# Kernel optimization log

Measured on AMD Instinct MI355X. Metric: run time of the kernel, lower is better.

Reference implementation:

```python
import jax, jax.numpy as jnp
import numpy as np

N, E, H, NH, S, EF, K = 25000, 400000, 64, 4, 16, 8, 2
HS = H // NH  # head size


def _ln(x, w, b):
    m = x.mean(-1, keepdims=True)
    v = ((x - m) ** 2).mean(-1, keepdims=True)
    return (x - m) / jnp.sqrt(v + 1e-5) * w + b


def _seg_softmax(scores, seg, n):
    # scores: [E, NH], seg: [E] -> softmax over edges sharing the same dest node
    mx = jax.ops.segment_max(scores, seg, num_segments=n)
    e = jnp.exp(scores - mx[seg])
    s = jax.ops.segment_sum(e, seg, num_segments=n)
    return e / (s[seg] + 1e-9)


def _edge_layer(h, x_s, src, dest, ef, w1, w2, proj, gated):
    # h: [N,H] (already layer-normed). Gather, fused per-edge MLP (no bias).
    inp = jnp.concatenate([h[src], h[dest], x_s[src], x_s[dest], ef], axis=-1)  # [E,168]
    raw = jnp.maximum(inp @ w1.T, 0.0) @ w2.T  # [E,NH]
    if gated:
        w = jax.nn.sigmoid(raw)
    else:
        w = _seg_softmax(jax.nn.leaky_relu(raw) / jnp.sqrt(jnp.asarray(HS, raw.dtype)), dest, N)
    msg = h.reshape(N, NH, HS)[src] * w[:, :, None]          # [E,NH,HS]
    agg = jax.ops.segment_sum(msg, dest, num_segments=N)     # [N,NH,HS]
    return agg.reshape(N, H) @ proj.T, w


def _mlp(x, w1, b1, w2, b2):
    return jnp.maximum(x @ w1.T + b1, 0.0) @ w2.T + b2


def _forward(x, x_s, edge_features, fwd_w1, fwd_w2, fwd_proj, rev_w1, rev_w2, rev_proj,
             ln_w, ln_b, r_w1, r_b1, r_w2, r_b2, z_w1, z_b1, z_w2, z_b2,
             c_w1, c_b1, c_w2, c_b2, edge_index):
    src, dest = edge_index[0], edge_index[1]
    # forward-direction stacked attention hops
    h_fwd, fwd_ws = x, []
    for k in range(K):
        h_norm = _ln(h_fwd, ln_w, ln_b)
        msg, w = _edge_layer(h_norm, x_s, src, dest, edge_features,
                             fwd_w1[k], fwd_w2[k], fwd_proj[k], gated=False)
        h_fwd = h_fwd + msg
        fwd_ws.append(w)
    fwd_ws = jnp.stack(fwd_ws, axis=-1)  # [E,NH,K]
    # reverse-direction stacked gating hops (edge direction flipped)
    h_rev, rev_ws = x, []
    for k in range(K):
        h_norm = _ln(h_rev, ln_w, ln_b)
        msg, w = _edge_layer(h_norm, x_s, dest, src, edge_features,
                             rev_w1[k], rev_w2[k], rev_proj[k], gated=True)
        h_rev = h_rev + msg
        rev_ws.append(w)
    rev_ws = jnp.stack(rev_ws, axis=-1)  # [E,NH,K]
    messages = jnp.concatenate([h_fwd - x, h_rev - x], axis=-1)  # [N,2H]
    gate_input = jnp.concatenate([x, messages], axis=-1)          # [N,3H]
    r_gate = jax.nn.sigmoid(_mlp(gate_input, r_w1, r_b1, r_w2, r_b2))
    z_gate = jax.nn.sigmoid(_mlp(gate_input, z_w1, z_b1, z_w2, z_b2))
    cand_in = jnp.concatenate([r_gate * x, messages], axis=-1)
    cand = jnp.tanh(_mlp(cand_in, c_w1, c_b1, c_w2, c_b2))
    final_h = (1.0 - z_gate) * x + z_gate * cand
    return final_h, fwd_ws, rev_ws, z_gate, r_gate


def setup_inputs() -> dict:
    key = jax.random.key(0)
    ks = jax.random.split(key, 20)
    mlp_in = 2 * H + 2 * S + EF  # 168
    width = 2 * H                # 128
    gi, gw = 3 * H, 3 * H        # 192, 192

    def nrm(k, shape, fan_in):
        return jax.random.normal(k, shape, jnp.float32) / np.sqrt(fan_in)

    return {
        'x': jax.random.normal(ks[0], (N, H), jnp.float32),
        'x_s': jax.random.normal(ks[1], (N, S), jnp.float32),
        'edge_index': jax.random.randint(ks[2], (2, E), 0, N, jnp.int32),
        'edge_features': jax.random.normal(ks[3], (E, EF), jnp.float32),
        'fwd_w1': nrm(ks[4], (K, width, mlp_in), mlp_in),
        'fwd_w2': nrm(ks[5], (K, NH, width), width),
        'fwd_proj': nrm(ks[6], (K, H, H), H),
        'rev_w1': nrm(ks[7], (K, width, mlp_in), mlp_in),
        'rev_w2': nrm(ks[8], (K, NH, width), width),
        'rev_proj': nrm(ks[9], (K, H, H), H),
        'ln_w': jnp.ones((H,), jnp.float32),
        'ln_b': jnp.zeros((H,), jnp.float32),
        'r_w1': nrm(ks[10], (gw, gi), gi), 'r_b1': jnp.zeros((gw,), jnp.float32),
        'r_w2': nrm(ks[11], (H, gw), gw), 'r_b2': jnp.zeros((H,), jnp.float32),
        'z_w1': nrm(ks[12], (gw, gi), gi), 'z_b1': jnp.zeros((gw,), jnp.float32),
        'z_w2': nrm(ks[13], (H, gw), gw), 'z_b2': jnp.zeros((H,), jnp.float32),
        'c_w1': nrm(ks[14], (gw, gi), gi), 'c_b1': jnp.zeros((gw,), jnp.float32),
        'c_w2': nrm(ks[15], (H, gw), gw), 'c_b2': jnp.zeros((H,), jnp.float32),
    }


def reference(x, x_s, edge_index, edge_features, fwd_w1, fwd_w2, fwd_proj,
              rev_w1, rev_w2, rev_proj, ln_w, ln_b, r_w1, r_b1, r_w2, r_b2,
              z_w1, z_b1, z_w2, z_b2, c_w1, c_b1, c_w2, c_b2):
    return _forward(x, x_s, edge_features, fwd_w1, fwd_w2, fwd_proj,
                    rev_w1, rev_w2, rev_proj, ln_w, ln_b,
                    r_w1, r_b1, r_w2, r_b2, z_w1, z_b1, z_w2, z_b2,
                    c_w1, c_b1, c_w2, c_b2, edge_index)
```

## Files before the change

### kernel.cpp

```cpp
#include <hip/hip_runtime.h>
#include <hip/hip_fp16.h>
#include <math.h>

#define NN 25000
#define EE 400000
#define HH 64
#define NHEAD 4
#define SDIM 16
#define EFDIM 8
#define KHOP 2
#define MIN 168
#define WID 128
#define GIN 192
#define KP 96

typedef __attribute__((ext_vector_type(8))) short bf16x8;
typedef __attribute__((ext_vector_type(4))) float f32x4;
typedef unsigned short ushortT;
typedef unsigned int uintT;

__device__ __forceinline__ float wave_sum64(float v) {
#pragma unroll
  for (int m = 1; m <= 32; m <<= 1) v += __shfl_xor(v, m, 64);
  return v;
}

__device__ __forceinline__ ushortT f2b(float f) {
  uintT u = __float_as_uint(f);
  return (ushortT)((u + 0x7FFFu + ((u >> 16) & 1u)) >> 16);
}
__device__ __forceinline__ float b2f(ushortT h) {
  return __uint_as_float(((uintT)h) << 16);
}

union U4H8 {
  uint4 u;
  __half2 h[4];
};

__device__ __forceinline__ __half2 relu2(__half2 v) {
  union { __half2 h; uintT u; } x;
  x.h = v;
  uintT mask = ((x.u & 0x80008000u) >> 15) * 0xFFFFu;
  x.u &= ~mask;
  return x.h;
}

__global__ void k_histo2(const int* __restrict__ src, const int* __restrict__ dst,
                         int* __restrict__ cnt_s, int* __restrict__ cnt_d) {
  int e = blockIdx.x * 256 + threadIdx.x;
  if (e < EE) {
    atomicAdd(&cnt_d[dst[e]], 1);
    atomicAdd(&cnt_s[src[e]], 1);
  }
}

__global__ void k_scan2(const int* __restrict__ cnt_d, const int* __restrict__ cnt_s,
                        int* __restrict__ rp_d, int* __restrict__ rp_s) {
  const int* cnt = blockIdx.x ? cnt_s : cnt_d;
  int* rp = blockIdx.x ? rp_s : rp_d;
  __shared__ int part[1024];
  int t = threadIdx.x;
  const int CH = (NN + 1023) / 1024;
  int base = t * CH;
  int s = 0;
  for (int i = 0; i < CH; ++i) {
    int j = base + i;
    if (j < NN) s += cnt[j];
  }
  part[t] = s;
  __syncthreads();
  for (int off = 1; off < 1024; off <<= 1) {
    int v = (t >= off) ? part[t - off] : 0;
    __syncthreads();
    part[t] += v;
    __syncthreads();
  }
  int run = (t == 0) ? 0 : part[t - 1];
  for (int i = 0; i < CH; ++i) {
    int j = base + i;
    if (j < NN) { rp[j] = run; run += cnt[j]; }
  }
  if (t == 1023) rp[NN] = run;
}

__global__ void k_scatter2(const int* __restrict__ src, const int* __restrict__ dst,
                           const int* __restrict__ rp_s, const int* __restrict__ rp_d,
                           int* __restrict__ cur_s, int* __restrict__ cur_d,
                           int* __restrict__ eid_s, int* __restrict__ eid_d) {
  int e = blockIdx.x * 256 + threadIdx.x;
  if (e < EE) {
    int nd = dst[e];
    int pd = atomicAdd(&cur_d[nd], 1);
    eid_d[rp_d[nd] + pd] = e;
    int ns = src[e];
    int ps = atomicAdd(&cur_s[ns], 1);
    eid_s[rp_s[ns] + ps] = e;
  }
}

__global__ __launch_bounds__(256) void k_sortseg2(const int* __restrict__ rp_d,
                                                  const int* __restrict__ rp_s,
                                                  int* __restrict__ eid_d,
                                                  int* __restrict__ eid_s) {
  int gw = blockIdx.x * 4 + (threadIdx.x >> 6);
  int lane = threadIdx.x & 63;
  if (gw >= 2 * NN) return;
  const int* rp = (gw < NN) ? rp_d : rp_s;
  int* eids = (gw < NN) ? eid_d : eid_s;
  int node = (gw < NN) ? gw : gw - NN;
  int beg = rp[node], end = rp[node + 1];
  int deg = end - beg;
  if (deg <= 1) return;
  if (deg <= 64) {
    int v = (lane < deg) ? eids[beg + lane] : 0x7fffffff;
#pragma unroll
    for (int k = 2; k <= 64; k <<= 1) {
#pragma unroll
      for (int j = k >> 1; j > 0; j >>= 1) {
        int other = __shfl_xor(v, j, 64);
        bool takeMin = (((lane & k) == 0) == ((lane & j) == 0));
        v = takeMin ? min(v, other) : max(v, other);
      }
    }
    if (lane < deg) eids[beg + lane] = v;
  } else if (lane == 0) {
    for (int i = beg + 1; i < end; ++i) {
      int v = eids[i];
      int j = i - 1;
      while (j >= beg && eids[j] > v) { eids[j + 1] = eids[j]; --j; }
      eids[j + 1] = v;
    }
  }
}

__global__ void k_mkpos2(const int* __restrict__ eid_d, const int* __restrict__ eid_s,
                         const int* __restrict__ src, const int* __restrict__ dst,
                         const float* __restrict__ ef, int4* __restrict__ pos_f,
                         int4* __restrict__ pos_r, uint4* __restrict__ efh_f,
                         uint4* __restrict__ efh_r) {
  int i = blockIdx.x * 256 + threadIdx.x;
  if (i >= EE) return;
  int e1 = eid_d[i];
  pos_f[i] = make_int4(e1, src[e1], dst[e1], 0);
  int e2 = eid_s[i];
  pos_r[i] = make_int4(e2, dst[e2], src[e2], 0);
  {
    float4 a0 = *(const float4*)(ef + (size_t)e1 * EFDIM);
    float4 a1 = *(const float4*)(ef + (size_t)e1 * EFDIM + 4);
    U4H8 u;
    u.h[0] = __floats2half2_rn(a0.x, a0.y);
    u.h[1] = __floats2half2_rn(a0.z, a0.w);
    u.h[2] = __floats2half2_rn(a1.x, a1.y);
    u.h[3] = __floats2half2_rn(a1.z, a1.w);
    efh_f[i] = u.u;
  }
  {
    float4 b0 = *(const float4*)(ef + (size_t)e2 * EFDIM);
    float4 b1 = *(const float4*)(ef + (size_t)e2 * EFDIM + 4);
    U4H8 u;
    u.h[0] = __floats2half2_rn(b0.x, b0.y);
    u.h[1] = __floats2half2_rn(b0.z, b0.w);
    u.h[2] = __floats2half2_rn(b1.x, b1.y);
    u.h[3] = __floats2half2_rn(b1.z, b1.w);
    efh_r[i] = u.u;
  }
}

#define PACKN (256 * KP + 512 + 256 + 4096)
__global__ void k_pack_bf(const float* __restrict__ fw1, const float* __restrict__ rw1,
                          const float* __restrict__ fw2, const float* __restrict__ rw2,
                          const float* __restrict__ fpj, const float* __restrict__ rpj,
                          ushortT* __restrict__ pAB_all, __half2* __restrict__ w1e2_all,
                          __half2* __restrict__ w22_all, ushortT* __restrict__ pj_all) {
  int y = blockIdx.y;
  const float* w1 = (y < 2) ? fw1 + (size_t)y * WID * MIN
                            : rw1 + (size_t)(y - 2) * WID * MIN;
  const float* w2 = (y < 2) ? fw2 + (size_t)y * NHEAD * WID
                            : rw2 + (size_t)(y - 2) * NHEAD * WID;
  const float* pj = (y < 2) ? fpj + (size_t)y * HH * HH
                            : rpj + (size_t)(y - 2) * HH * HH;
  int i = blockIdx.x * 256 + threadIdx.x;
  if (i < 256 * KP) {
    int j = i / KP, k = i % KP;
    float v = 0.f;
    if (k < 80) {
      int row = (j < 128) ? j : j - 128;
      int col = (j < 128) ? (k < 64 ? k : k + 64) : (k < 64 ? k + 64 : k + 80);
      v = w1[row * MIN + col];
    }
    pAB_all[(size_t)y * 256 * KP + i] = f2b(v);
  } else if (i < 256 * KP + 512) {
    int jj = i - 256 * KP;
    int f = jj >> 6, jp = jj & 63;
    w1e2_all[y * 512 + jj] =
        __floats2half2_rn(w1[(2 * jp) * MIN + 160 + f], w1[(2 * jp + 1) * MIN + 160 + f]);
  } else if (i < 256 * KP + 512 + 256) {
    int jj = i - 256 * KP - 512;
    int o = jj >> 6, jp = jj & 63;
    w22_all[y * 256 + jj] = __floats2half2_rn(w2[o * WID + 2 * jp], w2[o * WID + 2 * jp + 1]);
  } else if (i < PACKN) {
    int jj = i - 256 * KP - 512 - 256;
    pj_all[y * 4096 + jj] = f2b(pj[jj]);
  }
}

#define CW1 (GIN * GIN)
#define CW2 (HH * GIN)
__global__ void k_cvt6(const float* __restrict__ r_w1, const float* __restrict__ z_w1,
                       const float* __restrict__ c_w1, const float* __restrict__ r_w2,
                       const float* __restrict__ z_w2, const float* __restrict__ c_w2,
                       ushortT* __restrict__ rzw1, ushortT* __restrict__ cw1,
                       ushortT* __restrict__ rw2, ushortT* __restrict__ zw2,
                       ushortT* __restrict__ cw2) {
  int i = blockIdx.x * 256 + threadIdx.x;
  if (i < CW1) rzw1[i] = f2b(r_w1[i]);
  else if (i < 2 * CW1) rzw1[i] = f2b(z_w1[i - CW1]);
  else if (i < 3 * CW1) cw1[i - 2 * CW1] = f2b(c_w1[i - 2 * CW1]);
  else if (i < 3 * CW1 + CW2) rw2[i - 3 * CW1] = f2b(r_w2[i - 3 * CW1]);
  else if (i < 3 * CW1 + 2 * CW2) zw2[i - 3 * CW1 - CW2] = f2b(z_w2[i - 3 * CW1 - CW2]);
  else if (i < 3 * CW1 + 3 * CW2) cw2[i - 3 * CW1 - 2 * CW2] = f2b(c_w2[i - 3 * CW1 - 2 * CW2]);
}

__global__ __launch_bounds__(256) void k_ln_init(
    const float* __restrict__ x, const float* __restrict__ xs,
    const float* __restrict__ lw, const float* __restrict__ lb,
    ushortT* __restrict__ ncf0, ushortT* __restrict__ ncr0,
    ushortT* __restrict__ ncf1, ushortT* __restrict__ ncr1) {
  int t = threadIdx.x;
  int node = blockIdx.x * 4 + (t >> 6), lane = t & 63;
  if (node >= NN) return;
  float v = x[(size_t)node * HH + lane];
  float mean = wave_sum64(v) * (1.0f / 64.0f);
  float d = v - mean;
  float var = wave_sum64(d * d) * (1.0f / 64.0f);
  ushortT val = f2b(d * rsqrtf(var + 1e-5f) * lw[lane] + lb[lane]);
  ncf0[(size_t)node * KP + lane] = val;
  ncr0[(size_t)node * KP + lane] = val;
  if (lane < SDIM) {
    ushortT xv = f2b(xs[(size_t)node * SDIM + lane]);
    ncf0[(size_t)node * KP + HH + lane] = xv;
    ncr0[(size_t)node * KP + HH + lane] = xv;
    ncf1[(size_t)node * KP + HH + lane] = xv;
    ncr1[(size_t)node * KP + HH + lane] = xv;
    ncf0[(size_t)node * KP + 80 + lane] = 0;
    ncr0[(size_t)node * KP + 80 + lane] = 0;
    ncf1[(size_t)node * KP + 80 + lane] = 0;
    ncr1[(size_t)node * KP + 80 + lane] = 0;
  }
}

__global__ __launch_bounds__(256) void k_proj2(
    const ushortT* __restrict__ Af, const ushortT* __restrict__ Ar,
    const ushortT* __restrict__ Wf, const ushortT* __restrict__ Wr,
    ushortT* __restrict__ Cf, ushortT* __restrict__ Cr) {
  int dir = blockIdx.y & 1;
  int n0 = (blockIdx.y >> 1) * 64;
  const ushortT* A = dir ? Ar : Af;
  const ushortT* W = dir ? Wr : Wf;
  ushortT* C = dir ? Cr : Cf;
  int w = threadIdx.x >> 6, l = threadIdx.x & 63;
  int m0 = blockIdx.x * 64 + w * 16;
  int rowa = m0 + (l & 15);
  int kb = l >> 4;
  bf16x8 afr0 = {0,0,0,0,0,0,0,0}, afr1 = afr0, afr2 = afr0;
  if (rowa < NN) {
    const ushortT* ap = A + (size_t)rowa * KP + kb * 8;
    afr0 = *(const bf16x8*)(ap);
    afr1 = *(const bf16x8*)(ap + 32);
    afr2 = *(const bf16x8*)(ap + 64);
  }
  int crow = m0 + (l >> 4) * 4;
  int ccol0 = l & 15;
  f32x4 acc[4];
#pragma unroll
  for (int n = 0; n < 4; ++n) acc[n] = (f32x4){0.f, 0.f, 0.f, 0.f};
  const ushortT* wbase = W + (size_t)(n0 + (l & 15)) * KP + kb * 8;
#pragma unroll
  for (int n = 0; n < 4; ++n) {
    const ushortT* wp = wbase + (size_t)(16 * n) * KP;
    acc[n] = __builtin_amdgcn_mfma_f32_16x16x32_bf16(afr0, *(const bf16x8*)(wp), acc[n], 0, 0, 0);
    acc[n] = __builtin_amdgcn_mfma_f32_16x16x32_bf16(afr1, *(const bf16x8*)(wp + 32), acc[n], 0, 0, 0);
    acc[n] = __builtin_amdgcn_mfma_f32_16x16x32_bf16(afr2, *(const bf16x8*)(wp + 64), acc[n], 0, 0, 0);
  }
#pragma unroll
  for (int n = 0; n < 4; ++n) {
    int col = n0 + ccol0 + n * 16;
#pragma unroll
    for (int r = 0; r < 4; ++r) {
      int row = crow + r;
      if (row < NN)
        C[(size_t)row * 256 + col] = __half_as_ushort(__float2half(acc[n][r]));
    }
  }
}

template <int ACT, int BF16OUT, int KD>
__global__ __launch_bounds__(64) void k_gemm3(
    const ushortT* __restrict__ A, int lda, const ushortT* __restrict__ W,
    const float* __restrict__ bias, void* __restrict__ Cout, int ldc, int M,
    const float* __restrict__ zv, const float* __restrict__ xp) {
  constexpr int KS = KD / 32;
  int l = threadIdx.x;
  int m0 = blockIdx.x * 16;
  int n0 = blockIdx.y * 64;
  int rowa = m0 + (l & 15);
  int kb = l >> 4;
  bf16x8 afr[KS];
#pragma unroll
  for (int ks = 0; ks < KS; ++ks) {
    afr[ks] = (bf16x8){0, 0, 0, 0, 0, 0, 0, 0};
    if (rowa < M) afr[ks] = *(const bf16x8*)(A + (size_t)rowa * lda + ks * 32 + kb * 8);
  }
  f32x4 acc[4];
#pragma unroll
  for (int n = 0; n < 4; ++n) acc[n] = (f32x4){0.f, 0.f, 0.f, 0.f};
  const ushortT* wbase = W + (size_t)(n0 + (l & 15)) * KD + kb * 8;
#pragma unroll
  for (int n = 0; n < 4; ++n) {
    const ushortT* wp = wbase + (size_t)(16 * n) * KD;
#pragma unroll
    for (int ks = 0; ks < KS; ++ks)
      acc[n] = __builtin_amdgcn_mfma_f32_16x16x32_bf16(afr[ks], *(const bf16x8*)(wp + ks * 32),
                                                       acc[n], 0, 0, 0);
  }
  int crow = m0 + (l >> 4) * 4;
  int ccol0 = n0 + (l & 15);
#pragma unroll
  for (int n = 0; n < 4; ++n) {
    int col = ccol0 + n * 16;
    float bv = bias ? bias[col] : 0.f;
#pragma unroll
    for (int r = 0; r < 4; ++r) {
      int row = crow + r;
      if (row < M) {
        float v = acc[n][r] + bv;
        if (ACT == 1) v = fmaxf(v, 0.f);
        else if (ACT == 2) v = 1.f / (1.f + expf(-v));
        else if (ACT == 3) v = tanhf(v);
        else if (ACT == 5) {
          float z = zv[(size_t)row * HH + col];
          float xv = xp[(size_t)row * HH + col];
          v = (1.f - z) * xv + z * tanhf(v);
        }
        if (BF16OUT)
          ((ushortT*)Cout)[(size_t)row * ldc + col] = f2b(v);
        else
          ((float*)Cout)[(size_t)row * ldc + col] = v;
      }
    }
  }
}

__global__ __launch_bounds__(64) void k_gemm_rz3(
    const ushortT* __restrict__ hid, const ushortT* __restrict__ rw2,
    const ushortT* __restrict__ zw2, const float* __restrict__ rb2,
    const float* __restrict__ zb2, float* __restrict__ outR, float* __restrict__ outZ,
    const float* __restrict__ x, ushortT* __restrict__ gi) {
  int y = blockIdx.y;
  const ushortT* A = hid + (y ? GIN : 0);
  const ushortT* W = y ? zw2 : rw2;
  const float* bias = y ? zb2 : rb2;
  float* C = y ? outZ : outR;
  constexpr int KS = GIN / 32;
  int l = threadIdx.x;
  int m0 = blockIdx.x * 16;
  int rowa = m0 + (l & 15);
  int kb = l >> 4;
  bf16x8 afr[KS];
#pragma unroll
  for (int ks = 0; ks < KS; ++ks) {
    afr[ks] = (bf16x8){0, 0, 0, 0, 0, 0, 0, 0};
    if (rowa < NN) afr[ks] = *(const bf16x8*)(A + (size_t)rowa * 384 + ks * 32 + kb * 8);
  }
  f32x4 acc[4];
#pragma unroll
  for (int n = 0; n < 4; ++n) acc[n] = (f32x4){0.f, 0.f, 0.f, 0.f};
  const ushortT* wbase = W + (size_t)(l & 15) * GIN + kb * 8;
#pragma unroll
  for (int n = 0; n < 4; ++n) {
    const ushortT* wp = wbase + (size_t)(16 * n) * GIN;
#pragma unroll
    for (int ks = 0; ks < KS; ++ks)
      acc[n] = __builtin_amdgcn_mfma_f32_16x16x32_bf16(afr[ks], *(const bf16x8*)(wp + ks * 32),
                                                       acc[n], 0, 0, 0);
  }
  int crow = m0 + (l >> 4) * 4;
  int ccol0 = l & 15;
#pragma unroll
  for (int n = 0; n < 4; ++n) {
    int col = ccol0 + n * 16;
    float bv = bias[col];
#pragma unroll
    for (int r = 0; r < 4; ++r) {
      int row = crow + r;
      if (row < NN) {
        float v = acc[n][r] + bv;
        float sig = 1.f / (1.f + expf(-v));
        C[(size_t)row * HH + col] = sig;
        if (y == 0)
          gi[(size_t)row * GIN + col] = f2b(sig * x[(size_t)row * HH + col]);
      }
    }
  }
}

__global__ __launch_bounds__(256) void k_edge3(
    const ushortT* __restrict__ cABf, const ushortT* __restrict__ cABr,
    const int4* __restrict__ pos_f, const int4* __restrict__ pos_r,
    const uint4* __restrict__ efh_f, const uint4* __restrict__ efh_r,
    const __half2* __restrict__ w1e2_f, const __half2* __restrict__ w1e2_r,
    const __half2* __restrict__ w22_f, const __half2* __restrict__ w22_r,
    float* __restrict__ s_seq, float* __restrict__ outRW,
    float* __restrict__ ws_seq, int hop) {
  int y = blockIdx.y;
  const __half2* cAB2 = (const __half2*)(y ? cABr : cABf);
  const int4* pos = y ? pos_r : pos_f;
  const uint4* efh = y ? efh_r : efh_f;
  const __half2* w1e2 = y ? w1e2_r : w1e2_f;
  const __half2* w22 = y ? w22_r : w22_f;
  __shared__ __half2 w1e2_s[8][64];
  __shared__ __half2 w22_s[4][64];
  int t = threadIdx.x;
  for (int i = t; i < 512; i += 256) w1e2_s[i >> 6][i & 63] = w1e2[i];
  if (t < 256) w22_s[t >> 6][t & 63] = w22[t];
  __syncthreads();
  int es = t >> 2, q = t & 3;
  size_t ii = (size_t)blockIdx.x * 64 + es;
  int4 pr = pos[ii];
  const __half2* cA2 = cAB2 + (size_t)pr.y * 128;
  const __half2* cB2 = cAB2 + (size_t)pr.z * 128 + 64;
  U4H8 efu;
  efu.u = efh[ii];
  __half2 efb[8];
#pragma unroll
  for (int f2v = 0; f2v < 4; ++f2v) {
    efb[2 * f2v] = __half2half2(__low2half(efu.h[f2v]));
    efb[2 * f2v + 1] = __half2half2(__high2half(efu.h[f2v]));
  }
  float pf[4] = {0.f, 0.f, 0.f, 0.f};
#pragma unroll
  for (int c = 0; c < 4; ++c) {
    int jp0 = c * 16 + q * 4;
    U4H8 ua, ub;
    ua.u = *(const uint4*)(cA2 + jp0);
    ub.u = *(const uint4*)(cB2 + jp0);
    __half2 h2v[4];
#pragma unroll
    for (int i2 = 0; i2 < 4; ++i2) h2v[i2] = __hadd2(ua.h[i2], ub.h[i2]);
#pragma unroll
    for (int f = 0; f < 8; ++f) {
      U4H8 wv;
      wv.u = *(const uint4*)(&w1e2_s[f][jp0]);
#pragma unroll
      for (int i2 = 0; i2 < 4; ++i2) h2v[i2] = __hfma2(efb[f], wv.h[i2], h2v[i2]);
    }
#pragma unroll
    for (int i2 = 0; i2 < 4; ++i2) h2v[i2] = relu2(h2v[i2]);
#pragma unroll
    for (int o = 0; o < 4; ++o) {
      U4H8 wv;
      wv.u = *(const uint4*)(&w22_s[o][jp0]);
      __half2 p2 = __hmul2(h2v[0], wv.h[0]);
      p2 = __hfma2(h2v[1], wv.h[1], p2);
      p2 = __hfma2(h2v[2], wv.h[2], p2);
      p2 = __hfma2(h2v[3], wv.h[3], p2);
      pf[o] += __low2float(p2) + __high2float(p2);
    }
  }
#pragma unroll
  for (int m = 1; m <= 2; m <<= 1) {
    pf[0] += __shfl_xor(pf[0], m, 64);
    pf[1] += __shfl_xor(pf[1], m, 64);
    pf[2] += __shfl_xor(pf[2], m, 64);
    pf[3] += __shfl_xor(pf[3], m, 64);
  }
  float pv = (q == 0) ? pf[0] : (q == 1) ? pf[1] : (q == 2) ? pf[2] : pf[3];
  if (y) {
    float sig = 1.f / (1.f + expf(-pv));
    outRW[(size_t)pr.x * (NHEAD * KHOP) + q * KHOP + hop] = sig;
    ws_seq[ii * 4 + q] = sig;
  } else {
    s_seq[ii * 4 + q] = (pv > 0.f ? pv : 0.01f * pv) * 0.25f;
  }
}

__global__ __launch_bounds__(256) void k_softagg5(
    const ushortT* __restrict__ ncf, const ushortT* __restrict__ ncr,
    const float* __restrict__ s_seq, const float* __restrict__ ws_seq, int hop,
    const int* __restrict__ rp_d, const int* __restrict__ rp_s,
    const int4* __restrict__ pos_f, const int4* __restrict__ pos_r,
    ushortT* __restrict__ agg_f, ushortT* __restrict__ agg_r,
    float* __restrict__ wout) {
  int y = blockIdx.y;
  const ushortT* hn_bf = y ? ncr : ncf;
  const int* rp = y ? rp_s : rp_d;
  const int4* pos = y ? pos_r : pos_f;
  ushortT* agg = y ? agg_r : agg_f;
  __shared__ float w_s[4][64][4];
  __shared__ int ot_s[4][64];
  int t = threadIdx.x;
  int wvi = t >> 6, lane = t & 63;
  int node = blockIdx.x * 4 + wvi;
  if (node >= NN) return;
  int beg = rp[node], end = rp[node + 1];
  int deg = end - beg;
  bool small = (deg <= 64);
  float mxv = 0.f, invv = 0.f;
  int li = lane >> 2, o = lane & 3;
  if (deg > 0 && small) {
    int i0 = beg + li;
    if (y == 0) {
      int ee4[4];
      float sv[4];
#pragma unroll
      for (int u = 0; u < 4; ++u) {
        int idx = i0 + u * 16;
        bool val = idx < end;
        int4 pr = pos[val ? idx : beg];
        ee4[u] = pr.x;
        if (o == 0 && val) ot_s[wvi][li + u * 16] = pr.y * KP;
        float v = s_seq[(size_t)(val ? idx : beg) * 4 + o];
        sv[u] = val ? v : -1e30f;
      }
      float mx = fmaxf(fmaxf(sv[0], sv[1]), fmaxf(sv[2], sv[3]));
#pragma unroll
      for (int m = 4; m <= 32; m <<= 1) mx = fmaxf(mx, __shfl_xor(mx, m, 64));
      float ex[4];
      float sum = 0.f;
#pragma unroll
      for (int u = 0; u < 4; ++u) {
        ex[u] = (sv[u] > -1e29f) ? expf(sv[u] - mx) : 0.f;
        sum += ex[u];
      }
#pragma unroll
      for (int m = 4; m <= 32; m <<= 1) sum += __shfl_xor(sum, m, 64);
      float inv = 1.f / (sum + 1e-9f);
#pragma unroll
      for (int u = 0; u < 4; ++u) {
        if (i0 + u * 16 < end) {
          float wv = ex[u] * inv;
          wout[(size_t)ee4[u] * (NHEAD * KHOP) + o * KHOP + hop] = wv;
          w_s[wvi][li + u * 16][o] = wv;
        }
      }
    } else {
#pragma unroll
      for (int u = 0; u < 4; ++u) {
        int idx = i0 + u * 16;
        bool val = idx < end;
        if (val) {
          if (o == 0) {
            int4 pr = pos[idx];
            ot_s[wvi][li + u * 16] = pr.y * KP;
          }
          w_s[wvi][li + u * 16][o] = ws_seq[(size_t)idx * 4 + o];
        }
      }
    }
  } else if (deg > 0) {
    if (y == 0) {
      float mx = -1e30f;
      for (int ii = beg + li; ii < end; ii += 16)
        mx = fmaxf(mx, s_seq[(size_t)ii * 4 + o]);
#pragma unroll
      for (int m = 4; m <= 32; m <<= 1) mx = fmaxf(mx, __shfl_xor(mx, m, 64));
      float sum = 0.f;
      for (int ii = beg + li; ii < end; ii += 16)
        sum += expf(s_seq[(size_t)ii * 4 + o] - mx);
#pragma unroll
      for (int m = 4; m <= 32; m <<= 1) sum += __shfl_xor(sum, m, 64);
      float inv = 1.f / (sum + 1e-9f);
      for (int ii = beg + li; ii < end; ii += 16) {
        wout[(size_t)pos[ii].x * (NHEAD * KHOP) + o * KHOP + hop] =
            expf(s_seq[(size_t)ii * 4 + o] - mx) * inv;
      }
      mxv = mx;
      invv = inv;
    }
  }
  int hd = lane >> 4;
  float acc = 0.f;
  if (small) {
    for (int ii = 0; ii < deg; ii += 8) {
#pragma unroll
      for (int u = 0; u < 8; ++u) {
        int ed = ii + u;
        int edc = (ed < deg) ? ed : 0;
        int ot = ot_s[wvi][edc];
        float w = w_s[wvi][edc][hd];
        float hv = b2f(hn_bf[(size_t)ot + lane]);
        acc += ((ed < deg) ? w : 0.f) * hv;
      }
    }
  } else {
    float mx_hd = 0.f, inv_hd = 0.f;
    if (y == 0) {
      mx_hd = __shfl(mxv, hd, 64);
      inv_hd = __shfl(invv, hd, 64);
    }
    for (int ii = beg; ii < end; ++ii) {
      int4 pr = pos[ii];
      float w;
      if (y == 0)
        w = expf(s_seq[(size_t)ii * 4 + hd] - mx_hd) * inv_hd;
      else
        w = ws_seq[(size_t)ii * 4 + hd];
      acc += w * b2f(hn_bf[(size_t)pr.y * KP + lane]);
    }
  }
  agg[(size_t)node * HH + lane] = f2b(acc);
}

template <int DO_LN, int DO_GATE>
__global__ __launch_bounds__(64) void k_projout(
    const ushortT* __restrict__ agg_f, const ushortT* __restrict__ agg_r,
    const ushortT* __restrict__ pj_f, const ushortT* __restrict__ pj_r,
    float* __restrict__ h_f, float* __restrict__ h_r,
    ushortT* __restrict__ ncf_n, ushortT* __restrict__ ncr_n,
    const float* __restrict__ lnw, const float* __restrict__ lnb,
    const float* __restrict__ x, ushortT* __restrict__ gi) {
  int y = blockIdx.y;
  const ushortT* A = y ? agg_r : agg_f;
  const ushortT* W = y ? pj_r : pj_f;
  float* h = y ? h_r : h_f;
  ushortT* ncat_n = y ? ncr_n : ncf_n;
  int l = threadIdx.x;
  int m0 = blockIdx.x * 16;
  int rowa = m0 + (l & 15);
  int kb = l >> 4;
  bf16x8 afr0 = {0, 0, 0, 0, 0, 0, 0, 0}, afr1 = afr0;
  if (rowa < NN) {
    afr0 = *(const bf16x8*)(A + (size_t)rowa * HH + kb * 8);
    afr1 = *(const bf16x8*)(A + (size_t)rowa * HH + 32 + kb * 8);
  }
  f32x4 acc[4];
#pragma unroll
  for (int n = 0; n < 4; ++n) acc[n] = (f32x4){0.f, 0.f, 0.f, 0.f};
  const ushortT* wbase = W + (size_t)(l & 15) * HH + kb * 8;
#pragma unroll
  for (int n = 0; n < 4; ++n) {
    const ushortT* wp = wbase + (size_t)(16 * n) * HH;
    acc[n] = __builtin_amdgcn_mfma_f32_16x16x32_bf16(afr0, *(const bf16x8*)(wp), acc[n], 0, 0, 0);
    acc[n] = __builtin_amdgcn_mfma_f32_16x16x32_bf16(afr1, *(const bf16x8*)(wp + 32), acc[n], 0, 0, 0);
  }
  int crow = m0 + (l >> 4) * 4;
  int ccol0 = l & 15;
#pragma unroll
  for (int r = 0; r < 4; ++r) {
    int row = crow + r;
    if (row >= NN) continue;
    float hv[4];
#pragma unroll
    for (int n = 0; n < 4; ++n)
      hv[n] = h[(size_t)row * HH + ccol0 + n * 16] + acc[n][r];
    float s = hv[0] + hv[1] + hv[2] + hv[3];
#pragma unroll
    for (int m = 1; m <= 8; m <<= 1) s += __shfl_xor(s, m, 64);
    float mean = s * (1.0f / 64.0f);
    float ss = 0.f;
#pragma unroll
    for (int n = 0; n < 4; ++n) {
      float d = hv[n] - mean;
      ss += d * d;
    }
#pragma unroll
    for (int m = 1; m <= 8; m <<= 1) ss += __shfl_xor(ss, m, 64);
    float rstd = rsqrtf(ss * (1.0f / 64.0f) + 1e-5f);
#pragma unroll
    for (int n = 0; n < 4; ++n) {
      int col = ccol0 + n * 16;
      size_t g = (size_t)row * HH + col;
      h[g] = hv[n];
      if (DO_LN)
        ncat_n[(size_t)row * KP + col] = f2b((hv[n] - mean) * rstd * lnw[col] + lnb[col]);
      if (DO_GATE) {
        float xv = x[g];
        if (y == 0) {
          gi[(size_t)row * GIN + col] = f2b(xv);
          gi[(size_t)row * GIN + 64 + col] = f2b(hv[n] - xv);
        } else {
          gi[(size_t)row * GIN + 128 + col] = f2b(hv[n] - xv);
        }
      }
    }
  }
}

extern "C" void kernel_launch(void* const* d_in, const int* in_sizes, int n_in,
                              void* d_out, int out_size, void* d_ws, size_t ws_size,
                              hipStream_t stream) {
  const float* x = (const float*)d_in[0];
  const float* xs = (const float*)d_in[1];
  const int* ei = (const int*)d_in[2];
  const float* ef = (const float*)d_in[3];
  const float* fw1 = (const float*)d_in[4];
  const float* fw2 = (const float*)d_in[5];
  const float* fpj = (const float*)d_in[6];
  const float* rw1 = (const float*)d_in[7];
  const float* rw2 = (const float*)d_in[8];
  const float* rpj = (const float*)d_in[9];
  const float* lnw = (const float*)d_in[10];
  const float* lnb = (const float*)d_in[11];
  const float* r_w1 = (const float*)d_in[12];
  const float* r_b1 = (const float*)d_in[13];
  const float* r_w2 = (const float*)d_in[14];
  const float* r_b2 = (const float*)d_in[15];
  const float* z_w1 = (const float*)d_in[16];
  const float* z_b1 = (const float*)d_in[17];
  const float* z_w2 = (const float*)d_in[18];
  const float* z_b2 = (const float*)d_in[19];
  const float* c_w1 = (const float*)d_in[20];
  const float* c_b1 = (const float*)d_in[21];
  const float* c_w2 = (const float*)d_in[22];
  const float* c_b2 = (const float*)d_in[23];
  const int* srcp = ei;
  const int* dstp = ei + EE;

  float* outF = (float*)d_out;
  float* outFW = outF + (size_t)NN * HH;
  float* outRW = outFW + (size_t)EE * NHEAD * KHOP;
  float* outZ = outRW + (size_t)EE * NHEAD * KHOP;
  float* outR = outZ + (size_t)NN * HH;

  char* Wb = (char*)d_ws;
  size_t off = 0;
  auto alloc = [&](size_t bytes) -> void* {
    void* p = Wb + off;
    off += (bytes + 255) & ~(size_t)255;
    return p;
  };
  float* h_fwd = (float*)alloc((size_t)NN * HH * 4);
  float* h_rev = (float*)alloc((size_t)NN * HH * 4);
  ushortT* ncat_f0 = (ushortT*)alloc((size_t)NN * KP * 2);
  ushortT* ncat_r0 = (ushortT*)alloc((size_t)NN * KP * 2);
  ushortT* ncat_f1 = (ushortT*)alloc((size_t)NN * KP * 2);
  ushortT* ncat_r1 = (ushortT*)alloc((size_t)NN * KP * 2);
  float* s_seq = (float*)alloc((size_t)EE * NHEAD * 4);
  float* ws_seq = (float*)alloc((size_t)EE * NHEAD * 4);
  char* big = (char*)alloc((size_t)2 * NN * 256 * 2);
  ushortT* cAB_f = (ushortT*)big;
  ushortT* cAB_r = (ushortT*)(big + (size_t)NN * 256 * 2);
  ushortT* hid_bf = (ushortT*)big;
  ushortT* gi_bf = (ushortT*)alloc((size_t)NN * GIN * 2);
  ushortT* agg_f = (ushortT*)alloc((size_t)NN * HH * 2);
  ushortT* agg_r = (ushortT*)alloc((size_t)NN * HH * 2);
  ushortT* packAB_bf = (ushortT*)alloc((size_t)4 * 256 * KP * 2);
  __half2* w1e2h = (__half2*)alloc((size_t)4 * 512 * 4);
  __half2* w22h = (__half2*)alloc((size_t)4 * 256 * 4);
  ushortT* pj_bf = (ushortT*)alloc((size_t)4 * 4096 * 2);
  ushortT* rzw1_bf = (ushortT*)alloc((size_t)384 * GIN * 2);
  ushortT* rw2_bf = (ushortT*)alloc((size_t)HH * GIN * 2);
  ushortT* zw2_bf = (ushortT*)alloc((size_t)HH * GIN * 2);
  ushortT* cw1_bf = (ushortT*)alloc((size_t)GIN * GIN * 2);
  ushortT* cw2_bf = (ushortT*)alloc((size_t)HH * GIN * 2);
  float* rz_b1 = (float*)alloc(384 * 4);
  int* rp_d = (int*)alloc((NN + 8) * 4);
  int* rp_s = (int*)alloc((NN + 8) * 4);
  int* cur2 = (int*)alloc((size_t)2 * NN * 4);
  int* cur_d = cur2;
  int* cur_s = cur2 + NN;
  int* eid_d = (int*)alloc((size_t)EE * 4);
  int* eid_s = (int*)alloc((size_t)EE * 4);
  int4* pos_f = (int4*)alloc((size_t)EE * 16);
  int4* pos_r = (int4*)alloc((size_t)EE * 16);
  uint4* efh_f = (uint4*)alloc((size_t)EE * 16);
  uint4* efh_r = (uint4*)alloc((size_t)EE * 16);

  (void)hipMemcpyAsync(h_fwd, x, (size_t)NN * HH * 4, hipMemcpyDeviceToDevice, stream);
  (void)hipMemcpyAsync(h_rev, x, (size_t)NN * HH * 4, hipMemcpyDeviceToDevice, stream);
  (void)hipMemcpyAsync(rz_b1, r_b1, GIN * 4, hipMemcpyDeviceToDevice, stream);
  (void)hipMemcpyAsync(rz_b1 + GIN, z_b1, GIN * 4, hipMemcpyDeviceToDevice, stream);

  const int EB = (EE + 255) / 256, NW = (NN + 3) / 4;
  const int PB = (PACKN + 255) / 256;

  dim3 gPack(PB, 4);
  k_pack_bf<<<gPack, 256, 0, stream>>>(fw1, rw1, fw2, rw2, fpj, rpj, packAB_bf,
                                       w1e2h, w22h, pj_bf);
  k_cvt6<<<(3 * CW1 + 3 * CW2 + 255) / 256, 256, 0, stream>>>(
      r_w1, z_w1, c_w1, r_w2, z_w2, c_w2, rzw1_bf, cw1_bf, rw2_bf, zw2_bf, cw2_bf);

  (void)hipMemsetAsync(cur2, 0, (size_t)2 * NN * 4, stream);
  k_histo2<<<EB, 256, 0, stream>>>(srcp, dstp, cur_s, cur_d);
  k_scan2<<<2, 1024, 0, stream>>>(cur_d, cur_s, rp_d, rp_s);
  (void)hipMemsetAsync(cur2, 0, (size_t)2 * NN * 4, stream);
  k_scatter2<<<EB, 256, 0, stream>>>(srcp, dstp, rp_s, rp_d, cur_s, cur_d, eid_s, eid_d);
  k_sortseg2<<<(2 * NN + 3) / 4, 256, 0, stream>>>(rp_d, rp_s, eid_d, eid_s);
  k_mkpos2<<<EB, 256, 0, stream>>>(eid_d, eid_s, srcp, dstp, ef, pos_f, pos_r, efh_f, efh_r);

  k_ln_init<<<NW, 256, 0, stream>>>(x, xs, lnw, lnb, ncat_f0, ncat_r0, ncat_f1, ncat_r1);

  const int MB64 = (NN + 63) / 64;
  const int MB16 = (NN + 15) / 16;
  dim3 gProj(MB64, 8), gEdge(EE / 64, 2), gAgg(NW, 2), gPO(MB16, 2);
  for (int k = 0; k < KHOP; ++k) {
    const ushortT* nf = k ? ncat_f1 : ncat_f0;
    const ushortT* nr = k ? ncat_r1 : ncat_r0;
    k_proj2<<<gProj, 256, 0, stream>>>(nf, nr,
                                       packAB_bf + (size_t)k * 256 * KP,
                                       packAB_bf + (size_t)(2 + k) * 256 * KP,
                                       cAB_f, cAB_r);
    k_edge3<<<gEdge, 256, 0, stream>>>(cAB_f, cAB_r, pos_f, pos_r, efh_f, efh_r,
                                       w1e2h + (size_t)k * 512,
                                       w1e2h + (size_t)(2 + k) * 512,
                                       w22h + (size_t)k * 256,
                                       w22h + (size_t)(2 + k) * 256,
                                       s_seq, outRW, ws_seq, k);
    k_softagg5<<<gAgg, 256, 0, stream>>>(nf, nr, s_seq, ws_seq, k, rp_d, rp_s,
                                         pos_f, pos_r, agg_f, agg_r, outFW);
    if (k == 0)
      k_projout<1, 0><<<gPO, 64, 0, stream>>>(
          agg_f, agg_r, pj_bf + (size_t)k * 4096, pj_bf + (size_t)(2 + k) * 4096,
          h_fwd, h_rev, ncat_f1, ncat_r1, lnw, lnb, x, gi_bf);
    else
      k_projout<0, 1><<<gPO, 64, 0, stream>>>(
          agg_f, agg_r, pj_bf + (size_t)k * 4096, pj_bf + (size_t)(2 + k) * 4096,
          h_fwd, h_rev, ncat_f1, ncat_r1, lnw, lnb, x, gi_bf);
  }

  dim3 gRZ1(MB16, 6), gRZ2(MB16, 2), gC1(MB16, 3), gF(MB16, 1);
  k_gemm3<1, 1, GIN><<<gRZ1, 64, 0, stream>>>(gi_bf, GIN, rzw1_bf, rz_b1, hid_bf,
                                              384, NN, nullptr, nullptr);
  k_gemm_rz3<<<gRZ2, 64, 0, stream>>>(hid_bf, rw2_bf, zw2_bf, r_b2, z_b2, outR, outZ,
                                      x, gi_bf);
  k_gemm3<1, 1, GIN><<<gC1, 64, 0, stream>>>(gi_bf, GIN, cw1_bf, c_b1, hid_bf, GIN,
                                             NN, nullptr, nullptr);
  k_gemm3<5, 0, GIN><<<gF, 64, 0, stream>>>(hid_bf, GIN, cw2_bf, c_b2, outF, HH, NN,
                                            outZ, x);
}
```

Measured before the change: 498.6 us.

## Fuse per-edge MLP into node-centric softmax aggregation kernel

Merges the edge-scoring kernel into the per-destination softmax/aggregation kernel, so each wave computes edge MLP scores for its node's edges in registers and applies softmax and aggregation directly. This removes the round trip of per-edge scores through global memory and one launch. It also widens the cAB rows to hold the layer-normed node features next to the projected halves, so the aggregation gather reads from the same buffer. The trade-off is that per-edge MLP work is now tied to node degree, which can cause load imbalance, and it uses extra memory for the wider rows.

```diff
diff --git a/kernel.cpp b/kernel.cpp
--- a/kernel.cpp
+++ b/kernel.cpp
@@ -13,6 +13,7 @@
 #define WID 128
 #define GIN 192
 #define KP 96
+#define CROW 320
 
 typedef __attribute__((ext_vector_type(8))) short bf16x8;
 typedef __attribute__((ext_vector_type(4))) float f32x4;
@@ -226,7 +227,8 @@
     const float* __restrict__ x, const float* __restrict__ xs,
     const float* __restrict__ lw, const float* __restrict__ lb,
     ushortT* __restrict__ ncf0, ushortT* __restrict__ ncr0,
-    ushortT* __restrict__ ncf1, ushortT* __restrict__ ncr1) {
+    ushortT* __restrict__ ncf1, ushortT* __restrict__ ncr1,
+    ushortT* __restrict__ cABf, ushortT* __restrict__ cABr) {
   int t = threadIdx.x;
   int node = blockIdx.x * 4 + (t >> 6), lane = t & 63;
   if (node >= NN) return;
@@ -237,6 +239,8 @@
   ushortT val = f2b(d * rsqrtf(var + 1e-5f) * lw[lane] + lb[lane]);
   ncf0[(size_t)node * KP + lane] = val;
   ncr0[(size_t)node * KP + lane] = val;
+  cABf[(size_t)node * CROW + 256 + lane] = val;
+  cABr[(size_t)node * CROW + 256 + lane] = val;
   if (lane < SDIM) {
     ushortT xv = f2b(xs[(size_t)node * SDIM + lane]);
     ncf0[(size_t)node * KP + HH + lane] = xv;
@@ -290,7 +294,7 @@
     for (int r = 0; r < 4; ++r) {
       int row = crow + r;
       if (row < NN)
-        C[(size_t)row * 256 + col] = __half_as_ushort(__float2half(acc[n][r]));
+        C[(size_t)row * CROW + col] = __half_as_ushort(__float2half(acc[n][r]));
     }
   }
 }
@@ -405,33 +409,13 @@
   }
 }
 
-__global__ __launch_bounds__(256) void k_edge3(
-    const ushortT* __restrict__ cABf, const ushortT* __restrict__ cABr,
-    const int4* __restrict__ pos_f, const int4* __restrict__ pos_r,
-    const uint4* __restrict__ efh_f, const uint4* __restrict__ efh_r,
-    const __half2* __restrict__ w1e2_f, const __half2* __restrict__ w1e2_r,
-    const __half2* __restrict__ w22_f, const __half2* __restrict__ w22_r,
-    float* __restrict__ s_seq, float* __restrict__ outRW,
-    float* __restrict__ ws_seq, int hop) {
-  int y = blockIdx.y;
-  const __half2* cAB2 = (const __half2*)(y ? cABr : cABf);
-  const int4* pos = y ? pos_r : pos_f;
-  const uint4* efh = y ? efh_r : efh_f;
-  const __half2* w1e2 = y ? w1e2_r : w1e2_f;
-  const __half2* w22 = y ? w22_r : w22_f;
-  __shared__ __half2 w1e2_s[8][64];
-  __shared__ __half2 w22_s[4][64];
-  int t = threadIdx.x;
-  for (int i = t; i < 512; i += 256) w1e2_s[i >> 6][i & 63] = w1e2[i];
-  if (t < 256) w22_s[t >> 6][t & 63] = w22[t];
-  __syncthreads();
-  int es = t >> 2, q = t & 3;
-  size_t ii = (size_t)blockIdx.x * 64 + es;
-  int4 pr = pos[ii];
-  const __half2* cA2 = cAB2 + (size_t)pr.y * 128;
-  const __half2* cB2 = cAB2 + (size_t)pr.z * 128 + 64;
+__device__ __forceinline__ float edge_mlp(
+    const __half2* __restrict__ cAB2, int other, int owner, uint4 efraw,
+    const __half2 (*w1e2_s)[64], const __half2 (*w22_s)[64], int q) {
+  const __half2* cA2 = cAB2 + (size_t)other * (CROW / 2);
+  const __half2* cB2 = cAB2 + (size_t)owner * (CROW / 2) + 64;
   U4H8 efu;
-  efu.u = efh[ii];
+  efu.u = efraw;
   __half2 efb[8];
 #pragma unroll
   for (int f2v = 0; f2v < 4; ++f2v) {
@@ -475,54 +459,72 @@
     pf[2] += __shfl_xor(pf[2], m, 64);
     pf[3] += __shfl_xor(pf[3], m, 64);
   }
-  float pv = (q == 0) ? pf[0] : (q == 1) ? pf[1] : (q == 2) ? pf[2] : pf[3];
-  if (y) {
-    float sig = 1.f / (1.f + expf(-pv));
-    outRW[(size_t)pr.x * (NHEAD * KHOP) + q * KHOP + hop] = sig;
-    ws_seq[ii * 4 + q] = sig;
-  } else {
-    s_seq[ii * 4 + q] = (pv > 0.f ? pv : 0.01f * pv) * 0.25f;
-  }
-}
-
-__global__ __launch_bounds__(256) void k_softagg5(
-    const ushortT* __restrict__ ncf, const ushortT* __restrict__ ncr,
-    const float* __restrict__ s_seq, const float* __restrict__ ws_seq, int hop,
+  return (q == 0) ? pf[0] : (q == 1) ? pf[1] : (q == 2) ? pf[2] : pf[3];
+}
+
+__global__ __launch_bounds__(256) void k_edgeagg(
+    const ushortT* __restrict__ cABf, const ushortT* __restrict__ cABr,
+    const int4* __restrict__ pos_f, const int4* __restrict__ pos_r,
+    const uint4* __restrict__ efh_f, const uint4* __restrict__ efh_r,
+    const __half2* __restrict__ w1e2_f, const __half2* __restrict__ w1e2_r,
+    const __half2* __restrict__ w22_f, const __half2* __restrict__ w22_r,
     const int* __restrict__ rp_d, const int* __restrict__ rp_s,
-    const int4* __restrict__ pos_f, const int4* __restrict__ pos_r,
-    ushortT* __restrict__ agg_f, ushortT* __restrict__ agg_r,
-    float* __restrict__ wout) {
+    float* __restrict__ s_seq, float* __restrict__ ws_seq,
+    float* __restrict__ wout, float* __restrict__ outRW,
+    ushortT* __restrict__ agg_f, ushortT* __restrict__ agg_r, int hop) {
   int y = blockIdx.y;
-  const ushortT* hn_bf = y ? ncr : ncf;
+  const ushortT* cAB = y ? cABr : cABf;
+  const __half2* cAB2 = (const __half2*)cAB;
+  const int4* pos = y ? pos_r : pos_f;
+  const uint4* efh = y ? efh_r : efh_f;
+  const __half2* w1e2 = y ? w1e2_r : w1e2_f;
+  const __half2* w22 = y ? w22_r : w22_f;
   const int* rp = y ? rp_s : rp_d;
-  const int4* pos = y ? pos_r : pos_f;
   ushortT* agg = y ? agg_r : agg_f;
+  __shared__ __half2 w1e2_s[8][64];
+  __shared__ __half2 w22_s[4][64];
   __shared__ float w_s[4][64][4];
   __shared__ int ot_s[4][64];
   int t = threadIdx.x;
+  for (int i = t; i < 512; i += 256) w1e2_s[i >> 6][i & 63] = w1e2[i];
+  if (t < 256) w22_s[t >> 6][t & 63] = w22[t];
+  __syncthreads();
   int wvi = t >> 6, lane = t & 63;
   int node = blockIdx.x * 4 + wvi;
   if (node >= NN) return;
   int beg = rp[node], end = rp[node + 1];
   int deg = end - beg;
   bool small = (deg <= 64);
+  int li = lane >> 2, q = lane & 3;
   float mxv = 0.f, invv = 0.f;
-  int li = lane >> 2, o = lane & 3;
-  if (deg > 0 && small) {
-    int i0 = beg + li;
-    if (y == 0) {
-      int ee4[4];
-      float sv[4];
-#pragma unroll
-      for (int u = 0; u < 4; ++u) {
-        int idx = i0 + u * 16;
+
+  if (small) {
+    float sv[4];
+    int ee4[4];
+#pragma unroll
+    for (int u = 0; u < 4; ++u) { sv[u] = -1e30f; ee4[u] = 0; }
+#pragma unroll
+    for (int u = 0; u < 4; ++u) {
+      if (u * 16 < deg) {
+        int idx = beg + li + u * 16;
         bool val = idx < end;
-        int4 pr = pos[val ? idx : beg];
+        int idxc = val ? idx : beg;
+        int4 pr = pos[idxc];
         ee4[u] = pr.x;
-        if (o == 0 && val) ot_s[wvi][li + u * 16] = pr.y * KP;
-        float v = s_seq[(size_t)(val ? idx : beg) * 4 + o];
-        sv[u] = val ? v : -1e30f;
-      }
+        if (q == 0 && val) ot_s[wvi][li + u * 16] = pr.y;
+        float pv = edge_mlp(cAB2, pr.y, pr.z, efh[idxc], w1e2_s, w22_s, q);
+        if (y) {
+          float sig = 1.f / (1.f + expf(-pv));
+          if (val) {
+            outRW[(size_t)pr.x * (NHEAD * KHOP) + q * KHOP + hop] = sig;
+            w_s[wvi][li + u * 16][q] = sig;
+          }
+        } else {
+          sv[u] = val ? (pv > 0.f ? pv : 0.01f * pv) * 0.25f : -1e30f;
+        }
+      }
+    }
+    if (y == 0 && deg > 0) {
       float mx = fmaxf(fmaxf(sv[0], sv[1]), fmaxf(sv[2], sv[3]));
 #pragma unroll
       for (int m = 4; m <= 32; m <<= 1) mx = fmaxf(mx, __shfl_xor(mx, m, 64));
@@ -538,42 +540,40 @@
       float inv = 1.f / (sum + 1e-9f);
 #pragma unroll
       for (int u = 0; u < 4; ++u) {
-        if (i0 + u * 16 < end) {
+        if (beg + li + u * 16 < end) {
           float wv = ex[u] * inv;
-          wout[(size_t)ee4[u] * (NHEAD * KHOP) + o * KHOP + hop] = wv;
-          w_s[wvi][li + u * 16][o] = wv;
+          wout[(size_t)ee4[u] * (NHEAD * KHOP) + q * KHOP + hop] = wv;
+          w_s[wvi][li + u * 16][q] = wv;
         }
       }
-    } else {
-#pragma unroll
-      for (int u = 0; u < 4; ++u) {
-        int idx = i0 + u * 16;
-        bool val = idx < end;
-        if (val) {
-          if (o == 0) {
-            int4 pr = pos[idx];
-            ot_s[wvi][li + u * 16] = pr.y * KP;
-          }
-          w_s[wvi][li + u * 16][o] = ws_seq[(size_t)idx * 4 + o];
-        }
-      }
-    }
-  } else if (deg > 0) {
+    }
+  } else {
+    for (int ii = beg + li; ii < end; ii += 16) {
+      int4 pr = pos[ii];
+      float pv = edge_mlp(cAB2, pr.y, pr.z, efh[ii], w1e2_s, w22_s, q);
+      if (y) {
+        float sig = 1.f / (1.f + expf(-pv));
+        outRW[(size_t)pr.x * (NHEAD * KHOP) + q * KHOP + hop] = sig;
+        ws_seq[(size_t)ii * 4 + q] = sig;
+      } else {
+        s_seq[(size_t)ii * 4 + q] = (pv > 0.f ? pv : 0.01f * pv) * 0.25f;
+      }
+    }
     if (y == 0) {
       float mx = -1e30f;
       for (int ii = beg + li; ii < end; ii += 16)
-        mx = fmaxf(mx, s_seq[(size_t)ii * 4 + o]);
+        mx = fmaxf(mx, s_seq[(size_t)ii * 4 + q]);
 #pragma unroll
       for (int m = 4; m <= 32; m <<= 1) mx = fmaxf(mx, __shfl_xor(mx, m, 64));
       float sum = 0.f;
       for (int ii = beg + li; ii < end; ii += 16)
-        sum += expf(s_seq[(size_t)ii * 4 + o] - mx);
+        sum += expf(s_seq[(size_t)ii * 4 + q] - mx);
 #pragma unroll
       for (int m = 4; m <= 32; m <<= 1) sum += __shfl_xor(sum, m, 64);
       float inv = 1.f / (sum + 1e-9f);
       for (int ii = beg + li; ii < end; ii += 16) {
-        wout[(size_t)pos[ii].x * (NHEAD * KHOP) + o * KHOP + hop] =
-            expf(s_seq[(size_t)ii * 4 + o] - mx) * inv;
+        wout[(size_t)pos[ii].x * (NHEAD * KHOP) + q * KHOP + hop] =
+            expf(s_seq[(size_t)ii * 4 + q] - mx) * inv;
       }
       mxv = mx;
       invv = inv;
@@ -587,9 +587,9 @@
       for (int u = 0; u < 8; ++u) {
         int ed = ii + u;
         int edc = (ed < deg) ? ed : 0;
-        int ot = ot_s[wvi][edc];
+        size_t ot = (size_t)ot_s[wvi][edc] * CROW + 256;
         float w = w_s[wvi][edc][hd];
-        float hv = b2f(hn_bf[(size_t)ot + lane]);
+        float hv = b2f(cAB[ot + lane]);
         acc += ((ed < deg) ? w : 0.f) * hv;
       }
     }
@@ -606,7 +606,7 @@
         w = expf(s_seq[(size_t)ii * 4 + hd] - mx_hd) * inv_hd;
       else
         w = ws_seq[(size_t)ii * 4 + hd];
-      acc += w * b2f(hn_bf[(size_t)pr.y * KP + lane]);
+      acc += w * b2f(cAB[(size_t)pr.y * CROW + 256 + lane]);
     }
   }
   agg[(size_t)node * HH + lane] = f2b(acc);
@@ -618,6 +618,7 @@
     const ushortT* __restrict__ pj_f, const ushortT* __restrict__ pj_r,
     float* __restrict__ h_f, float* __restrict__ h_r,
     ushortT* __restrict__ ncf_n, ushortT* __restrict__ ncr_n,
+    ushortT* __restrict__ cABf, ushortT* __restrict__ cABr,
     const float* __restrict__ lnw, const float* __restrict__ lnb,
     const float* __restrict__ x, ushortT* __restrict__ gi) {
   int y = blockIdx.y;
@@ -625,6 +626,7 @@
   const ushortT* W = y ? pj_r : pj_f;
   float* h = y ? h_r : h_f;
   ushortT* ncat_n = y ? ncr_n : ncf_n;
+  ushortT* cab = y ? cABr : cABf;
   int l = threadIdx.x;
   int m0 = blockIdx.x * 16;
   int rowa = m0 + (l & 15);
@@ -672,8 +674,11 @@
       int col = ccol0 + n * 16;
       size_t g = (size_t)row * HH + col;
       h[g] = hv[n];
-      if (DO_LN)
-        ncat_n[(size_t)row * KP + col] = f2b((hv[n] - mean) * rstd * lnw[col] + lnb[col]);
+      if (DO_LN) {
+        ushortT val = f2b((hv[n] - mean) * rstd * lnw[col] + lnb[col]);
+        ncat_n[(size_t)row * KP + col] = val;
+        cab[(size_t)row * CROW + 256 + col] = val;
+      }
       if (DO_GATE) {
         float xv = x[g];
         if (y == 0) {
@@ -738,9 +743,9 @@
   ushortT* ncat_r1 = (ushortT*)alloc((size_t)NN * KP * 2);
   float* s_seq = (float*)alloc((size_t)EE * NHEAD * 4);
   float* ws_seq = (float*)alloc((size_t)EE * NHEAD * 4);
-  char* big = (char*)alloc((size_t)2 * NN * 256 * 2);
+  char* big = (char*)alloc((size_t)2 * NN * CROW * 2);
   ushortT* cAB_f = (ushortT*)big;
-  ushortT* cAB_r = (ushortT*)(big + (size_t)NN * 256 * 2);
+  ushortT* cAB_r = (ushortT*)(big + (size_t)NN * CROW * 2);
   ushortT* hid_bf = (ushortT*)big;
   ushortT* gi_bf = (ushortT*)alloc((size_t)NN * GIN * 2);
   ushortT* agg_f = (ushortT*)alloc((size_t)NN * HH * 2);
@@ -789,11 +794,12 @@
   k_sortseg2<<<(2 * NN + 3) / 4, 256, 0, stream>>>(rp_d, rp_s, eid_d, eid_s);
   k_mkpos2<<<EB, 256, 0, stream>>>(eid_d, eid_s, srcp, dstp, ef, pos_f, pos_r, efh_f, efh_r);
 
-  k_ln_init<<<NW, 256, 0, stream>>>(x, xs, lnw, lnb, ncat_f0, ncat_r0, ncat_f1, ncat_r1);
+  k_ln_init<<<NW, 256, 0, stream>>>(x, xs, lnw, lnb, ncat_f0, ncat_r0, ncat_f1,
+                                    ncat_r1, cAB_f, cAB_r);
 
   const int MB64 = (NN + 63) / 64;
   const int MB16 = (NN + 15) / 16;
-  dim3 gProj(MB64, 8), gEdge(EE / 64, 2), gAgg(NW, 2), gPO(MB16, 2);
+  dim3 gProj(MB64, 8), gEA(NW, 2), gPO(MB16, 2);
   for (int k = 0; k < KHOP; ++k) {
     const ushortT* nf = k ? ncat_f1 : ncat_f0;
     const ushortT* nr = k ? ncat_r1 : ncat_r0;
@@ -801,22 +807,21 @@
                                        packAB_bf + (size_t)k * 256 * KP,
                                        packAB_bf + (size_t)(2 + k) * 256 * KP,
                                        cAB_f, cAB_r);
-    k_edge3<<<gEdge, 256, 0, stream>>>(cAB_f, cAB_r, pos_f, pos_r, efh_f, efh_r,
+    k_edgeagg<<<gEA, 256, 0, stream>>>(cAB_f, cAB_r, pos_f, pos_r, efh_f, efh_r,
                                        w1e2h + (size_t)k * 512,
                                        w1e2h + (size_t)(2 + k) * 512,
                                        w22h + (size_t)k * 256,
                                        w22h + (size_t)(2 + k) * 256,
-                                       s_seq, outRW, ws_seq, k);
-    k_softagg5<<<gAgg, 256, 0, stream>>>(nf, nr, s_seq, ws_seq, k, rp_d, rp_s,
-                                         pos_f, pos_r, agg_f, agg_r, outFW);
+                                       rp_d, rp_s, s_seq, ws_seq, outFW, outRW,
+                                       agg_f, agg_r, k);
     if (k == 0)
       k_projout<1, 0><<<gPO, 64, 0, stream>>>(
           agg_f, agg_r, pj_bf + (size_t)k * 4096, pj_bf + (size_t)(2 + k) * 4096,
-          h_fwd, h_rev, ncat_f1, ncat_r1, lnw, lnb, x, gi_bf);
+          h_fwd, h_rev, ncat_f1, ncat_r1, cAB_f, cAB_r, lnw, lnb, x, gi_bf);
     else
       k_projout<0, 1><<<gPO, 64, 0, stream>>>(
           agg_f, agg_r, pj_bf + (size_t)k * 4096, pj_bf + (size_t)(2 + k) * 4096,
-          h_fwd, h_rev, ncat_f1, ncat_r1, lnw, lnb, x, gi_bf);
+          h_fwd, h_rev, ncat_f1, ncat_r1, cAB_f, cAB_r, lnw, lnb, x, gi_bf);
   }
 
   dim3 gRZ1(MB16, 6), gRZ2(MB16, 2), gC1(MB16, 3), gF(MB16, 1);
```

After: 778.0 us. 56.0% more time.
